# Performance work log

Hardware: AMD Instinct MI355X
Metric: run time of the kernel (lower is better)

The kernel has to match this reference:

```python
import jax, jax.numpy as jnp
import numpy as np

D_M, D_K, D_V, HEADS = 1024, 64, 64, 16
B, S = 2, 2048


def setup_inputs() -> dict:
    key = jax.random.key(0)
    ks = jax.random.split(key, 5)
    x = jax.random.normal(ks[0], (B, S, D_M), dtype=jnp.float32)
    # per-head projection weights (original deep-copies one rand init per head;
    # we give each head independent weights, matching the per-head param structure)
    Wk = jax.random.uniform(ks[1], (HEADS, D_M, D_K), dtype=jnp.float32)
    Wq = jax.random.uniform(ks[2], (HEADS, D_M, D_K), dtype=jnp.float32)
    Wv = jax.random.uniform(ks[3], (HEADS, D_M, D_V), dtype=jnp.float32)
    Wo = jax.random.uniform(ks[4], (HEADS * D_V, D_M), dtype=jnp.float32)
    return {"x": x, "Wk": Wk, "Wq": Wq, "Wv": Wv, "Wo": Wo}


def reference(x, Wk, Wq, Wv, Wo):
    # per-head QKV projections, batched over heads: [B,H,S,d]
    q = jnp.einsum("bsm,hmk->bhsk", x, Wq)
    k = jnp.einsum("bsm,hmk->bhsk", x, Wk)
    v = jnp.einsum("bsm,hmv->bhsv", x, Wv)
    scale = 1.0 / jnp.sqrt(jnp.asarray(q.shape[-1], dtype=q.dtype))
    scores = jnp.einsum("bhsk,bhtk->bhst", q, k) * scale  # [B,H,S,S]
    attn = jax.nn.softmax(scores, axis=-1)
    ctx = jnp.einsum("bhst,bhtv->bhsv", attn, v)  # [B,H,S,d_v]
    # concat heads -> [B,S,H*d_v], then output projection
    ctx = jnp.transpose(ctx, (0, 2, 1, 3)).reshape(x.shape[0], x.shape[1], -1)
    return jnp.einsum("bsc,cm->bsm", ctx, Wo)
```

## Files before the change

### kernel.cpp

```cpp
#include <hip/hip_runtime.h>
#include <hip/hip_bf16.h>
#include <stdint.h>

#define DM   1024
#define DKV  64
#define HEADS 16
#define BATCH 2
#define SEQ  2048
#define BS   (BATCH*SEQ)
#define BHD  (BATCH*HEADS)

typedef __attribute__((ext_vector_type(8))) short bf16x8;
typedef __attribute__((ext_vector_type(4))) short bf16x4;
typedef __attribute__((ext_vector_type(4))) float f32x4;

__device__ inline unsigned fb(float f) { union { float f; unsigned u; } v; v.f = f; return v.u; }

__device__ inline unsigned short bf16_rtn(float f) {
  unsigned u = fb(f);
  unsigned r = u + 0x7fffu + ((u >> 16) & 1u);
  return (unsigned short)(r >> 16);
}
__device__ inline float bf16_to_f(unsigned short h) {
  union { unsigned u; float f; } v; v.u = ((unsigned)h) << 16; return v.f;
}
__device__ inline void split_bf16(float x, unsigned short& hi, unsigned short& lo) {
  hi = bf16_rtn(x);
  lo = bf16_rtn(x - bf16_to_f(hi));
}
__device__ inline unsigned pack2_bf16(float lo_elem, float hi_elem) {
  return __builtin_amdgcn_perm(fb(hi_elem) + 0x8000u, fb(lo_elem) + 0x8000u, 0x07060302u);
}

__device__ inline float fast_exp2(float x) {
#if __has_builtin(__builtin_amdgcn_exp2f)
  return __builtin_amdgcn_exp2f(x);
#else
  return exp2f(x);
#endif
}

__device__ inline f32x4 mfma16x16x16_bf16(bf16x4 a, bf16x4 b, f32x4 c) {
#if __has_builtin(__builtin_amdgcn_mfma_f32_16x16x16bf16_1k)
  return __builtin_amdgcn_mfma_f32_16x16x16bf16_1k(a, b, c, 0, 0, 0);
#else
  asm volatile("v_mfma_f32_16x16x16_bf16 %0, %1, %2, %0" : "+v"(c) : "v"(a), "v"(b));
  return c;
#endif
}

__device__ inline void stage16(const unsigned short* g, unsigned short* lds_base, int lane) {
#if __has_builtin(__builtin_amdgcn_global_load_lds)
  __builtin_amdgcn_global_load_lds((__attribute__((address_space(1))) void*)(g),
                                   (__attribute__((address_space(3))) void*)(lds_base),
                                   16, 0, 0);
#else
  *(bf16x8*)(lds_base + lane * 8) = *(const bf16x8*)g;
#endif
}

__device__ inline int swz(int row, int chunk) {
  return row * 64 + (((chunk ^ (row & 7)) & 7) << 3);
}

__global__ void cvt_x_split(const float* __restrict__ x,
                            unsigned short* __restrict__ xh, unsigned short* __restrict__ xl) {
  int i = (blockIdx.x * 256 + threadIdx.x) * 8;
  bf16x8 oh, ol;
  #pragma unroll
  for (int j = 0; j < 8; ++j) {
    unsigned short hi, lo;
    split_bf16(x[i + j], hi, lo);
    oh[j] = (short)hi; ol[j] = (short)lo;
  }
  *(bf16x8*)(xh + i) = oh;
  *(bf16x8*)(xl + i) = ol;
}

__global__ void pack_qkv_split(const float* __restrict__ Wq, const float* __restrict__ Wk,
                               const float* __restrict__ Wv,
                               unsigned short* __restrict__ Wh, unsigned short* __restrict__ Wl) {
  __shared__ float tile[64][65];
  int bid = blockIdx.x;
  int p = bid >> 8, h = (bid >> 4) & 15, mt = bid & 15;
  const float* W = (p == 0) ? Wq : (p == 1) ? Wk : Wv;
  const float* src = W + (size_t)h * (DM * DKV);
  int t = threadIdx.x;
  int m0 = mt * 64;
  #pragma unroll
  for (int pass = 0; pass < 16; ++pass) {
    int row = pass * 4 + (t >> 6), col = t & 63;
    tile[row][col] = src[(size_t)(m0 + row) * DKV + col];
  }
  __syncthreads();
  int cbase = p * 1024 + h * 64;
  #pragma unroll
  for (int pass = 0; pass < 16; ++pass) {
    int krow = pass * 4 + (t >> 6), mcol = t & 63;
    unsigned short hi, lo;
    split_bf16(tile[mcol][krow], hi, lo);
    size_t idx = (size_t)(cbase + krow) * DM + m0 + mcol;
    Wh[idx] = hi; Wl[idx] = lo;
  }
}

__global__ void pack_wo(const float* __restrict__ Wo, unsigned short* __restrict__ WoT) {
  __shared__ float tile[64][65];
  int ib = blockIdx.x >> 4, jb = blockIdx.x & 15;
  int t = threadIdx.x;
  #pragma unroll
  for (int pass = 0; pass < 16; ++pass) {
    int row = pass * 4 + (t >> 6), col = t & 63;
    tile[row][col] = Wo[(size_t)(ib * 64 + row) * DM + jb * 64 + col];
  }
  __syncthreads();
  #pragma unroll
  for (int pass = 0; pass < 16; ++pass) {
    int a = pass * 4 + (t >> 6), b = t & 63;
    WoT[(size_t)(jb * 64 + a) * DM + ib * 64 + b] = bf16_rtn(tile[b][a]);
  }
}

__global__ __launch_bounds__(256, 2)
void gemm_qk(const unsigned short* __restrict__ Ah, const unsigned short* __restrict__ Al,
             const unsigned short* __restrict__ Bh, const unsigned short* __restrict__ Bl,
             unsigned short* __restrict__ Qh, unsigned short* __restrict__ Ql,
             unsigned short* __restrict__ Kh, unsigned short* __restrict__ Kl) {
  __shared__ unsigned short AsH[128 * 32], AsL[128 * 32];
  __shared__ unsigned short BsH[128 * 32], BsL[128 * 32];
  const int tid = threadIdx.x;
  const int w = tid >> 6, lane = tid & 63;
  const int quad = lane >> 4, l16 = lane & 15;
  const int wm = w >> 1, wn = w & 1;
  const int bn = blockIdx.x, bm = blockIdx.y;

  f32x4 acc[4][4];
  #pragma unroll
  for (int i = 0; i < 4; ++i)
    #pragma unroll
    for (int j = 0; j < 4; ++j) acc[i][j] = (f32x4){0.f, 0.f, 0.f, 0.f};

  const int r4 = lane >> 2, c4 = lane & 3;
  const size_t offA = (size_t)(bm * 128 + w * 32 + r4) * DM + c4 * 8;
  const size_t offB = (size_t)(bn * 128 + w * 32 + r4) * DM + c4 * 8;
  unsigned short* lAh0 = AsH + (w * 32) * 32;      unsigned short* lAh1 = AsH + (w * 32 + 16) * 32;
  unsigned short* lAl0 = AsL + (w * 32) * 32;      unsigned short* lAl1 = AsL + (w * 32 + 16) * 32;
  unsigned short* lBh0 = BsH + (w * 32) * 32;      unsigned short* lBh1 = BsH + (w * 32 + 16) * 32;
  unsigned short* lBl0 = BsL + (w * 32) * 32;      unsigned short* lBl1 = BsL + (w * 32 + 16) * 32;

  for (int kk = 0; kk < DM / 32; ++kk) {
    stage16(Ah + offA + kk * 32,           lAh0, lane);
    stage16(Ah + offA + kk * 32 + 16 * DM, lAh1, lane);
    stage16(Al + offA + kk * 32,           lAl0, lane);
    stage16(Al + offA + kk * 32 + 16 * DM, lAl1, lane);
    stage16(Bh + offB + kk * 32,           lBh0, lane);
    stage16(Bh + offB + kk * 32 + 16 * DM, lBh1, lane);
    stage16(Bl + offB + kk * 32,           lBl0, lane);
    stage16(Bl + offB + kk * 32 + 16 * DM, lBl1, lane);
    asm volatile("s_waitcnt vmcnt(0)" ::: "memory");
    __syncthreads();
    bf16x8 afh[4], afl[4], bfh[4], bfl[4];
    #pragma unroll
    for (int mt = 0; mt < 4; ++mt) {
      afh[mt] = *(const bf16x8*)(AsH + (wm * 64 + mt * 16 + l16) * 32 + quad * 8);
      afl[mt] = *(const bf16x8*)(AsL + (wm * 64 + mt * 16 + l16) * 32 + quad * 8);
    }
    #pragma unroll
    for (int nt = 0; nt < 4; ++nt) {
      bfh[nt] = *(const bf16x8*)(BsH + (wn * 64 + nt * 16 + l16) * 32 + quad * 8);
      bfl[nt] = *(const bf16x8*)(BsL + (wn * 64 + nt * 16 + l16) * 32 + quad * 8);
    }
    #pragma unroll
    for (int mt = 0; mt < 4; ++mt)
      #pragma unroll
      for (int nt = 0; nt < 4; ++nt) {
        acc[mt][nt] = __builtin_amdgcn_mfma_f32_16x16x32_bf16(afh[mt], bfh[nt], acc[mt][nt], 0, 0, 0);
        acc[mt][nt] = __builtin_amdgcn_mfma_f32_16x16x32_bf16(afh[mt], bfl[nt], acc[mt][nt], 0, 0, 0);
        acc[mt][nt] = __builtin_amdgcn_mfma_f32_16x16x32_bf16(afl[mt], bfh[nt], acc[mt][nt], 0, 0, 0);
      }
    __syncthreads();
  }

  const float SCL = 0.18033688011112042f;
  #pragma unroll
  for (int mt = 0; mt < 4; ++mt) {
    int m_g = bm * 128 + wm * 64 + mt * 16 + quad * 4;
    #pragma unroll
    for (int nt = 0; nt < 4; ++nt) {
      int n_g = bn * 128 + wn * 64 + nt * 16 + l16;
      int p = n_g >> 10, h = (n_g >> 6) & 15, k = n_g & 63;
      #pragma unroll
      for (int r = 0; r < 4; ++r) {
        int row = m_g + r;
        int b = row >> 11, s = row & 2047;
        int bh = b * HEADS + h;
        float v = acc[mt][nt][r];
        size_t idx = ((size_t)(bh * SEQ + s)) * DKV + k;
        unsigned short hi, lo;
        if (p == 0) {
          split_bf16(v * SCL, hi, lo);
          Qh[idx] = hi; Ql[idx] = lo;
        } else {
          split_bf16(v, hi, lo);
          Kh[idx] = hi; Kl[idx] = lo;
        }
      }
    }
  }
}

__global__ __launch_bounds__(256, 2)
void gemm_v(const unsigned short* __restrict__ A, const unsigned short* __restrict__ Bt,
            unsigned short* __restrict__ Vt) {
  __shared__ unsigned short As[128 * 32];
  __shared__ unsigned short Bs[128 * 32];
  const int tid = threadIdx.x;
  const int w = tid >> 6, lane = tid & 63;
  const int quad = lane >> 4, l16 = lane & 15;
  const int wm = w >> 1, wn = w & 1;
  const int bn = blockIdx.x, bm = blockIdx.y;

  f32x4 acc[4][4];
  #pragma unroll
  for (int i = 0; i < 4; ++i)
    #pragma unroll
    for (int j = 0; j < 4; ++j) acc[i][j] = (f32x4){0.f, 0.f, 0.f, 0.f};

  const int r4 = lane >> 2, c4 = lane & 3;
  const unsigned short* gA0 = A  + (size_t)(bm * 128 + w * 32 + r4) * DM + c4 * 8;
  const unsigned short* gB0 = Bt + (size_t)(bn * 128 + w * 32 + r4) * DM + c4 * 8;
  unsigned short* lA0 = As + (w * 32) * 32;
  unsigned short* lA1 = As + (w * 32 + 16) * 32;
  unsigned short* lB0 = Bs + (w * 32) * 32;
  unsigned short* lB1 = Bs + (w * 32 + 16) * 32;

  for (int kk = 0; kk < DM / 32; ++kk) {
    stage16(gA0 + kk * 32,           lA0, lane);
    stage16(gA0 + kk * 32 + 16 * DM, lA1, lane);
    stage16(gB0 + kk * 32,           lB0, lane);
    stage16(gB0 + kk * 32 + 16 * DM, lB1, lane);
    asm volatile("s_waitcnt vmcnt(0)" ::: "memory");
    __syncthreads();
    bf16x8 af[4], bfr[4];
    #pragma unroll
    for (int mt = 0; mt < 4; ++mt)
      af[mt] = *(const bf16x8*)(As + (wm * 64 + mt * 16 + l16) * 32 + quad * 8);
    #pragma unroll
    for (int nt = 0; nt < 4; ++nt)
      bfr[nt] = *(const bf16x8*)(Bs + (wn * 64 + nt * 16 + l16) * 32 + quad * 8);
    #pragma unroll
    for (int mt = 0; mt < 4; ++mt)
      #pragma unroll
      for (int nt = 0; nt < 4; ++nt)
        acc[mt][nt] = __builtin_amdgcn_mfma_f32_16x16x32_bf16(af[mt], bfr[nt], acc[mt][nt], 0, 0, 0);
    __syncthreads();
  }

  #pragma unroll
  for (int mt = 0; mt < 4; ++mt) {
    int m_g = bm * 128 + wm * 64 + mt * 16 + quad * 4;
    #pragma unroll
    for (int nt = 0; nt < 4; ++nt) {
      int n_g = bn * 128 + wn * 64 + nt * 16 + l16;
      int h = n_g >> 6, k = n_g & 63;
      #pragma unroll
      for (int r = 0; r < 4; ++r) {
        int row = m_g + r;
        int b = row >> 11, s = row & 2047;
        int bh = b * HEADS + h;
        Vt[((size_t)(bh * DKV + k)) * SEQ + s] = bf16_rtn(acc[mt][nt][r]);
      }
    }
  }
}

__global__ __launch_bounds__(256, 2)
void flash(const unsigned short* __restrict__ Qh, const unsigned short* __restrict__ Ql,
           const unsigned short* __restrict__ Kh, const unsigned short* __restrict__ Kl,
           const unsigned short* __restrict__ Vt, unsigned short* __restrict__ ctx) {
  __shared__ unsigned short KtH[64 * 64], KtL[64 * 64], Vts[64 * 64];
  const int tid = threadIdx.x;
  const int w = tid >> 6, lane = tid & 63, quad = lane >> 4, l16 = lane & 15;
  const int bh = blockIdx.x;
  const int q0 = blockIdx.y * 128;

  bf16x8 qfh[2][2], qfl[2][2];
  #pragma unroll
  for (int qt = 0; qt < 2; ++qt) {
    int qrow = q0 + w * 32 + qt * 16 + l16;
    size_t base = ((size_t)(bh * SEQ + qrow)) * DKV + quad * 8;
    qfh[qt][0] = *(const bf16x8*)(Qh + base);
    qfh[qt][1] = *(const bf16x8*)(Qh + base + 32);
    qfl[qt][0] = *(const bf16x8*)(Ql + base);
    qfl[qt][1] = *(const bf16x8*)(Ql + base + 32);
  }

  float m_run[2] = {-1e30f, -1e30f};
  float l_run[2] = {0.f, 0.f};
  f32x4 acc[2][4];
  #pragma unroll
  for (int qt = 0; qt < 2; ++qt)
    #pragma unroll
    for (int vt = 0; vt < 4; ++vt) acc[qt][vt] = (f32x4){0.f, 0.f, 0.f, 0.f};

  const int srow = tid >> 3, sc8 = tid & 7;

  bf16x8 rkh[2], rkl[2], rv[2];
  #pragma unroll
  for (int p = 0; p < 2; ++p) {
    int row = p * 32 + srow;
    size_t kidx = ((size_t)(bh * SEQ + row)) * DKV + sc8 * 8;
    rkh[p] = *(const bf16x8*)(Kh + kidx);
    rkl[p] = *(const bf16x8*)(Kl + kidx);
    rv[p]  = *(const bf16x8*)(Vt + ((size_t)(bh * DKV + row)) * SEQ + sc8 * 8);
  }

  for (int kt = 0; kt < SEQ / 64; ++kt) {
    __syncthreads();
    #pragma unroll
    for (int p = 0; p < 2; ++p) {
      int row = p * 32 + srow;
      int o = swz(row, sc8);
      *(bf16x8*)(KtH + o) = rkh[p];
      *(bf16x8*)(KtL + o) = rkl[p];
      *(bf16x8*)(Vts + o) = rv[p];
    }
    __syncthreads();
    if (kt + 1 < SEQ / 64) {
      int kt0 = (kt + 1) * 64;
      #pragma unroll
      for (int p = 0; p < 2; ++p) {
        int row = p * 32 + srow;
        size_t kidx = ((size_t)(bh * SEQ + kt0 + row)) * DKV + sc8 * 8;
        rkh[p] = *(const bf16x8*)(Kh + kidx);
        rkl[p] = *(const bf16x8*)(Kl + kidx);
        rv[p]  = *(const bf16x8*)(Vt + ((size_t)(bh * DKV + row)) * SEQ + kt0 + sc8 * 8);
      }
    }

    f32x4 st[4][2];
    #pragma unroll
    for (int mt = 0; mt < 4; ++mt) {
      int rowA = mt * 16 + l16;
      bf16x8 kah0 = *(const bf16x8*)(KtH + swz(rowA, quad));
      bf16x8 kah1 = *(const bf16x8*)(KtH + swz(rowA, quad + 4));
      bf16x8 kal0 = *(const bf16x8*)(KtL + swz(rowA, quad));
      bf16x8 kal1 = *(const bf16x8*)(KtL + swz(rowA, quad + 4));
      #pragma unroll
      for (int qt = 0; qt < 2; ++qt) {
        f32x4 c = (f32x4){0.f, 0.f, 0.f, 0.f};
        c = __builtin_amdgcn_mfma_f32_16x16x32_bf16(kah0, qfh[qt][0], c, 0, 0, 0);
        c = __builtin_amdgcn_mfma_f32_16x16x32_bf16(kah1, qfh[qt][1], c, 0, 0, 0);
        c = __builtin_amdgcn_mfma_f32_16x16x32_bf16(kah0, qfl[qt][0], c, 0, 0, 0);
        c = __builtin_amdgcn_mfma_f32_16x16x32_bf16(kah1, qfl[qt][1], c, 0, 0, 0);
        c = __builtin_amdgcn_mfma_f32_16x16x32_bf16(kal0, qfh[qt][0], c, 0, 0, 0);
        c = __builtin_amdgcn_mfma_f32_16x16x32_bf16(kal1, qfh[qt][1], c, 0, 0, 0);
        st[mt][qt] = c;
      }
    }

    bf16x4 pb[2][4];
    #pragma unroll
    for (int qt = 0; qt < 2; ++qt) {
      float cm = -1e30f;
      #pragma unroll
      for (int mt = 0; mt < 4; ++mt)
        #pragma unroll
        for (int r = 0; r < 4; ++r) cm = fmaxf(cm, st[mt][qt][r]);
      cm = fmaxf(cm, __shfl_xor(cm, 16));
      cm = fmaxf(cm, __shfl_xor(cm, 32));
      bool upd = cm > m_run[qt];
      float mn = upd ? cm : m_run[qt];
      float ssum = 0.f;
      #pragma unroll
      for (int mt = 0; mt < 4; ++mt) {
        float p0 = fast_exp2(st[mt][qt][0] - mn);
        float p1 = fast_exp2(st[mt][qt][1] - mn);
        float p2 = fast_exp2(st[mt][qt][2] - mn);
        float p3 = fast_exp2(st[mt][qt][3] - mn);
        ssum += (p0 + p1) + (p2 + p3);
        union { bf16x4 v; unsigned u2[2]; } pk;
        pk.u2[0] = pack2_bf16(p0, p1);
        pk.u2[1] = pack2_bf16(p2, p3);
        pb[qt][mt] = pk.v;
      }
      ssum += __shfl_xor(ssum, 16);
      ssum += __shfl_xor(ssum, 32);
      if (__ballot(upd)) {
        float alpha = fast_exp2(m_run[qt] - mn);
        m_run[qt] = mn;
        l_run[qt] = l_run[qt] * alpha + ssum;
        #pragma unroll
        for (int vt = 0; vt < 4; ++vt) acc[qt][vt] = acc[qt][vt] * alpha;
      } else {
        l_run[qt] += ssum;
      }
    }

    #pragma unroll
    for (int vt = 0; vt < 4; ++vt) {
      #pragma unroll
      for (int mt = 0; mt < 4; ++mt) {
        int row = vt * 16 + l16;
        int addr = row * 64 + ((((mt * 2 + (quad >> 1)) ^ (row & 7)) & 7) << 3) + (quad & 1) * 4;
        bf16x4 va = *(const bf16x4*)(Vts + addr);
        #pragma unroll
        for (int qt = 0; qt < 2; ++qt)
          acc[qt][vt] = mfma16x16x16_bf16(va, pb[qt][mt], acc[qt][vt]);
      }
    }
  }

  int h = bh & 15, b = bh >> 4;
  #pragma unroll
  for (int qt = 0; qt < 2; ++qt) {
    float inv = 1.0f / l_run[qt];
    int bs = b * SEQ + q0 + w * 32 + qt * 16 + l16;
    #pragma unroll
    for (int vt = 0; vt < 4; ++vt) {
      union { bf16x4 v; unsigned u2[2]; } pk;
      pk.u2[0] = pack2_bf16(acc[qt][vt][0] * inv, acc[qt][vt][1] * inv);
      pk.u2[1] = pack2_bf16(acc[qt][vt][2] * inv, acc[qt][vt][3] * inv);
      *(bf16x4*)(ctx + (size_t)bs * DM + h * 64 + vt * 16 + quad * 4) = pk.v;
    }
  }
}

__global__ __launch_bounds__(256, 2)
void gemm_out(const unsigned short* __restrict__ A, const unsigned short* __restrict__ Bt,
              float* __restrict__ out) {
  __shared__ unsigned short As[128 * 32];
  __shared__ unsigned short Bs[128 * 32];
  const int tid = threadIdx.x;
  const int w = tid >> 6, lane = tid & 63;
  const int quad = lane >> 4, l16 = lane & 15;
  const int wm = w >> 1, wn = w & 1;
  const int bn = blockIdx.x, bm = blockIdx.y;

  f32x4 acc[4][4];
  #pragma unroll
  for (int i = 0; i < 4; ++i)
    #pragma unroll
    for (int j = 0; j < 4; ++j) acc[i][j] = (f32x4){0.f, 0.f, 0.f, 0.f};

  const int r4 = lane >> 2, c4 = lane & 3;
  const unsigned short* gA0 = A  + (size_t)(bm * 128 + w * 32 + r4) * DM + c4 * 8;
  const unsigned short* gB0 = Bt + (size_t)(bn * 128 + w * 32 + r4) * DM + c4 * 8;
  unsigned short* lA0 = As + (w * 32) * 32;
  unsigned short* lA1 = As + (w * 32 + 16) * 32;
  unsigned short* lB0 = Bs + (w * 32) * 32;
  unsigned short* lB1 = Bs + (w * 32 + 16) * 32;

  for (int kk = 0; kk < DM / 32; ++kk) {
    stage16(gA0 + kk * 32,           lA0, lane);
    stage16(gA0 + kk * 32 + 16 * DM, lA1, lane);
    stage16(gB0 + kk * 32,           lB0, lane);
    stage16(gB0 + kk * 32 + 16 * DM, lB1, lane);
    asm volatile("s_waitcnt vmcnt(0)" ::: "memory");
    __syncthreads();
    bf16x8 af[4], bfr[4];
    #pragma unroll
    for (int mt = 0; mt < 4; ++mt)
      af[mt] = *(const bf16x8*)(As + (wm * 64 + mt * 16 + l16) * 32 + quad * 8);
    #pragma unroll
    for (int nt = 0; nt < 4; ++nt)
      bfr[nt] = *(const bf16x8*)(Bs + (wn * 64 + nt * 16 + l16) * 32 + quad * 8);
    #pragma unroll
    for (int mt = 0; mt < 4; ++mt)
      #pragma unroll
      for (int nt = 0; nt < 4; ++nt)
        acc[mt][nt] = __builtin_amdgcn_mfma_f32_16x16x32_bf16(af[mt], bfr[nt], acc[mt][nt], 0, 0, 0);
    __syncthreads();
  }

  #pragma unroll
  for (int mt = 0; mt < 4; ++mt) {
    int m_g = bm * 128 + wm * 64 + mt * 16 + quad * 4;
    #pragma unroll
    for (int nt = 0; nt < 4; ++nt) {
      int n_g = bn * 128 + wn * 64 + nt * 16 + l16;
      #pragma unroll
      for (int r = 0; r < 4; ++r)
        out[(size_t)(m_g + r) * DM + n_g] = acc[mt][nt][r];
    }
  }
}

extern "C" void kernel_launch(void* const* d_in, const int* in_sizes, int n_in,
                              void* d_out, int out_size, void* d_ws, size_t ws_size,
                              hipStream_t stream) {
  const float* x  = (const float*)d_in[0];
  const float* Wk = (const float*)d_in[1];
  const float* Wq = (const float*)d_in[2];
  const float* Wv = (const float*)d_in[3];
  const float* Wo = (const float*)d_in[4];
  float* out = (float*)d_out;

  unsigned short* xh  = (unsigned short*)d_ws;
  unsigned short* xl  = xh  + (size_t)BS * DM;
  unsigned short* Wh  = xl  + (size_t)BS * DM;
  unsigned short* Wl  = Wh  + (size_t)3 * DM * DM;
  unsigned short* WoT = Wl  + (size_t)3 * DM * DM;
  unsigned short* Qh  = WoT + (size_t)DM * DM;
  unsigned short* Ql  = Qh  + (size_t)BHD * SEQ * DKV;
  unsigned short* Kh  = Ql  + (size_t)BHD * SEQ * DKV;
  unsigned short* Kl  = Kh  + (size_t)BHD * SEQ * DKV;
  unsigned short* Vtb = Kl  + (size_t)BHD * SEQ * DKV;
  unsigned short* ctx = Vtb + (size_t)BHD * SEQ * DKV;

  cvt_x_split<<<(BS * DM) / (256 * 8), 256, 0, stream>>>(x, xh, xl);
  pack_qkv_split<<<3 * 16 * 16, 256, 0, stream>>>(Wq, Wk, Wv, Wh, Wl);
  pack_wo<<<16 * 16, 256, 0, stream>>>(Wo, WoT);
  gemm_qk<<<dim3(16, 32), 256, 0, stream>>>(xh, xl, Wh, Wl, Qh, Ql, Kh, Kl);
  gemm_v<<<dim3(8, 32), 256, 0, stream>>>(xh, Wh + (size_t)2048 * DM, Vtb);
  flash<<<dim3(BHD, SEQ / 128), 256, 0, stream>>>(Qh, Ql, Kh, Kl, Vtb, ctx);
  gemm_out<<<dim3(8, 32), 256, 0, stream>>>(ctx, WoT, out);
}
```

Before: 267.8 us.

## Double-buffer flash K/V tiles in LDS using direct global-to-LDS staging

New measurement: 272.1 us. Within noise of the previous version (+1.6%).

```diff
diff --git a/kernel.cpp b/kernel.cpp
--- a/kernel.cpp
+++ b/kernel.cpp
@@ -278,7 +278,7 @@
 void flash(const unsigned short* __restrict__ Qh, const unsigned short* __restrict__ Ql,
            const unsigned short* __restrict__ Kh, const unsigned short* __restrict__ Kl,
            const unsigned short* __restrict__ Vt, unsigned short* __restrict__ ctx) {
-  __shared__ unsigned short KtH[64 * 64], KtL[64 * 64], Vts[64 * 64];
+  __shared__ unsigned short KtH[2][64 * 64], KtL[2][64 * 64], Vts[2][64 * 64];
   const int tid = threadIdx.x;
   const int w = tid >> 6, lane = tid & 63, quad = lane >> 4, l16 = lane & 15;
   const int bh = blockIdx.x;
@@ -303,49 +303,45 @@
     #pragma unroll
     for (int vt = 0; vt < 4; ++vt) acc[qt][vt] = (f32x4){0.f, 0.f, 0.f, 0.f};
 
-  const int srow = tid >> 3, sc8 = tid & 7;
-
-  bf16x8 rkh[2], rkl[2], rv[2];
-  #pragma unroll
-  for (int p = 0; p < 2; ++p) {
-    int row = p * 32 + srow;
-    size_t kidx = ((size_t)(bh * SEQ + row)) * DKV + sc8 * 8;
-    rkh[p] = *(const bf16x8*)(Kh + kidx);
-    rkl[p] = *(const bf16x8*)(Kl + kidx);
-    rv[p]  = *(const bf16x8*)(Vt + ((size_t)(bh * DKV + row)) * SEQ + sc8 * 8);
-  }
+  const int srow = w * 16 + (lane >> 3);
+  const int csrc = (lane & 7) ^ (lane >> 3);
+  const unsigned short* kh_src = Kh + ((size_t)(bh * SEQ) + srow) * DKV + csrc * 8;
+  const unsigned short* kl_src = Kl + ((size_t)(bh * SEQ) + srow) * DKV + csrc * 8;
+  const unsigned short* v_src  = Vt + ((size_t)(bh * DKV) + srow) * SEQ + csrc * 8;
+
+  #define STAGE(buf, kt0)                                                     \
+    do {                                                                      \
+      unsigned short* dH = &KtH[buf][(w * 16) * 64];                          \
+      unsigned short* dL = &KtL[buf][(w * 16) * 64];                          \
+      unsigned short* dV = &Vts[buf][(w * 16) * 64];                          \
+      stage16(kh_src + (size_t)(kt0) * DKV,            dH,       lane);       \
+      stage16(kh_src + (size_t)(kt0) * DKV + 8 * DKV,  dH + 512, lane);       \
+      stage16(kl_src + (size_t)(kt0) * DKV,            dL,       lane);       \
+      stage16(kl_src + (size_t)(kt0) * DKV + 8 * DKV,  dL + 512, lane);       \
+      stage16(v_src  + (kt0),                          dV,       lane);       \
+      stage16(v_src  + (kt0) + 8 * SEQ,                dV + 512, lane);       \
+    } while (0)
+
+  STAGE(0, 0);
+  asm volatile("s_waitcnt vmcnt(0)" ::: "memory");
+  __syncthreads();
+  int cur = 0;
 
   for (int kt = 0; kt < SEQ / 64; ++kt) {
-    __syncthreads();
-    #pragma unroll
-    for (int p = 0; p < 2; ++p) {
-      int row = p * 32 + srow;
-      int o = swz(row, sc8);
-      *(bf16x8*)(KtH + o) = rkh[p];
-      *(bf16x8*)(KtL + o) = rkl[p];
-      *(bf16x8*)(Vts + o) = rv[p];
-    }
-    __syncthreads();
-    if (kt + 1 < SEQ / 64) {
-      int kt0 = (kt + 1) * 64;
-      #pragma unroll
-      for (int p = 0; p < 2; ++p) {
-        int row = p * 32 + srow;
-        size_t kidx = ((size_t)(bh * SEQ + kt0 + row)) * DKV + sc8 * 8;
-        rkh[p] = *(const bf16x8*)(Kh + kidx);
-        rkl[p] = *(const bf16x8*)(Kl + kidx);
-        rv[p]  = *(const bf16x8*)(Vt + ((size_t)(bh * DKV + row)) * SEQ + kt0 + sc8 * 8);
-      }
-    }
+    if (kt + 1 < SEQ / 64) STAGE(cur ^ 1, (kt + 1) * 64);
+
+    const unsigned short* kH = KtH[cur];
+    const unsigned short* kL = KtL[cur];
+    const unsigned short* vS = Vts[cur];
 
     f32x4 st[4][2];
     #pragma unroll
     for (int mt = 0; mt < 4; ++mt) {
       int rowA = mt * 16 + l16;
-      bf16x8 kah0 = *(const bf16x8*)(KtH + swz(rowA, quad));
-      bf16x8 kah1 = *(const bf16x8*)(KtH + swz(rowA, quad + 4));
-      bf16x8 kal0 = *(const bf16x8*)(KtL + swz(rowA, quad));
-      bf16x8 kal1 = *(const bf16x8*)(KtL + swz(rowA, quad + 4));
+      bf16x8 kah0 = *(const bf16x8*)(kH + swz(rowA, quad));
+      bf16x8 kah1 = *(const bf16x8*)(kH + swz(rowA, quad + 4));
+      bf16x8 kal0 = *(const bf16x8*)(kL + swz(rowA, quad));
+      bf16x8 kal1 = *(const bf16x8*)(kL + swz(rowA, quad + 4));
       #pragma unroll
       for (int qt = 0; qt < 2; ++qt) {
         f32x4 c = (f32x4){0.f, 0.f, 0.f, 0.f};
@@ -403,13 +399,18 @@
       for (int mt = 0; mt < 4; ++mt) {
         int row = vt * 16 + l16;
         int addr = row * 64 + ((((mt * 2 + (quad >> 1)) ^ (row & 7)) & 7) << 3) + (quad & 1) * 4;
-        bf16x4 va = *(const bf16x4*)(Vts + addr);
+        bf16x4 va = *(const bf16x4*)(vS + addr);
         #pragma unroll
         for (int qt = 0; qt < 2; ++qt)
           acc[qt][vt] = mfma16x16x16_bf16(va, pb[qt][mt], acc[qt][vt]);
       }
     }
-  }
+
+    asm volatile("s_waitcnt vmcnt(0)" ::: "memory");
+    __syncthreads();
+    cur ^= 1;
+  }
+  #undef STAGE
 
   int h = bh & 15, b = bh >> 4;
   #pragma unroll
```
